# Performance work log

Hardware: AMD Instinct MI355X
Metric: run time of the kernel (lower is better)

Reference implementation:

```python
import jax, jax.numpy as jnp
import numpy as np

EMBED = 1024
HEADS = 16
HEAD_DIM = EMBED // HEADS


def setup_inputs() -> dict:
    key = jax.random.key(0)
    ks = jax.random.split(key, 9)
    s = 0.02
    return {
        "hidden_states": jax.random.normal(ks[0], (1, 4, 1500, EMBED), dtype=jnp.float32),
        "q_w": jax.random.normal(ks[1], (EMBED, EMBED), dtype=jnp.float32) * s,
        "q_b": jax.random.normal(ks[2], (EMBED,), dtype=jnp.float32) * s,
        "k_w": jax.random.normal(ks[3], (EMBED, EMBED), dtype=jnp.float32) * s,
        "v_w": jax.random.normal(ks[4], (EMBED, EMBED), dtype=jnp.float32) * s,
        "v_b": jax.random.normal(ks[5], (EMBED,), dtype=jnp.float32) * s,
        "out_w": jax.random.normal(ks[6], (EMBED, EMBED), dtype=jnp.float32) * s,
        "out_b": jax.random.normal(ks[7], (EMBED,), dtype=jnp.float32) * s,
    }


def reference(hidden_states, q_w, q_b, k_w, v_w, v_b, out_w, out_b):
    # hidden_states: [1, B, S, E]
    _, bsz, tgt_len, _ = hidden_states.shape
    x = hidden_states[0]  # [B, S, E]
    scaling = HEAD_DIM ** -0.5

    def split_heads(t):  # [B, S, E] -> [B, H, S, Dh]
        return t.reshape(bsz, tgt_len, HEADS, HEAD_DIM).transpose(0, 2, 1, 3)

    # Linear layers use torch convention: y = x @ W.T + b  (k_proj has no bias)
    q = split_heads((x @ q_w.T + q_b) * scaling)
    k = split_heads(x @ k_w.T)
    v = split_heads(x @ v_w.T + v_b)

    # attention scores [B, H, S, S]
    attn_weights = jnp.einsum("bhqd,bhkd->bhqk", q, k)
    attn_probs = jax.nn.softmax(attn_weights, axis=-1)
    attn_out = jnp.einsum("bhqk,bhkd->bhqd", attn_probs, v)  # [B, H, S, Dh]

    attn_out = attn_out.transpose(0, 2, 1, 3).reshape(1, bsz, tgt_len, EMBED)
    return attn_out @ out_w.T + out_b
```

## Files before the change

### kernel.cpp

```cpp
#include <hip/hip_runtime.h>
#include <cstddef>
#include <cstdint>

#define EMB 1024
#define SEQ 1500
#define NB 4
#define NH 16
#define DH 64
#define MTOT (NB*SEQ)
#define VTS 1536

typedef __bf16 bf16;
typedef __bf16 bf16x4 __attribute__((ext_vector_type(4)));
typedef __bf16 bf16x8 __attribute__((ext_vector_type(8)));
typedef short  s16x4  __attribute__((ext_vector_type(4)));
typedef float  f32x4  __attribute__((ext_vector_type(4)));

#define LOG2E 1.44269504088896340736f

__device__ __forceinline__ void async16(const void* g, const void* l) {
    __builtin_amdgcn_global_load_lds(
        (const __attribute__((address_space(1))) uint32_t*)g,
        (__attribute__((address_space(3))) uint32_t*)l, 16, 0, 0);
}

__device__ __forceinline__ uint32_t pack_bf16_trunc(float e0, float e1) {
    return __builtin_amdgcn_perm(__builtin_bit_cast(uint32_t, e1),
                                 __builtin_bit_cast(uint32_t, e0), 0x07060302u);
}

struct CvtArgs {
    const float* xs; bf16* xd;
    const float* w[4]; bf16* wd[4];
};

__global__ __launch_bounds__(256) void cvt_kernel(CvtArgs a) {
    const size_t NX = (size_t)MTOT * EMB;
    const size_t NW = (size_t)EMB * EMB;
    const size_t tot = NX + 4 * NW;
    for (size_t i = ((size_t)blockIdx.x * 256 + threadIdx.x) * 4; i < tot;
         i += (size_t)gridDim.x * 1024) {
        const float* s; bf16* d; size_t off;
        if (i < NX) { s = a.xs; d = a.xd; off = i; }
        else {
            size_t j = i - NX;
            int wi = (int)(j >> 20);
            off = j & (NW - 1);
            s = a.w[wi]; d = a.wd[wi];
        }
        float4 v = *(const float4*)(s + off);
        bf16x4 o = { (bf16)v.x, (bf16)v.y, (bf16)v.z, (bf16)v.w };
        *(bf16x4*)(d + off) = o;
    }
}

__global__ __launch_bounds__(256) void gemm_fused(
    const bf16* __restrict__ X,
    const bf16* __restrict__ W0, const bf16* __restrict__ W1, const bf16* __restrict__ W2,
    const float* __restrict__ b_q, const float* __restrict__ b_v,
    bf16* __restrict__ Oq, bf16* __restrict__ Ok, bf16* __restrict__ Ovt,
    int M)
{
    __shared__ bf16 As[2][128 * 32];
    __shared__ bf16 Bs[2][128 * 32];
    const int tid = threadIdx.x;
    const int lane = tid & 63, w = tid >> 6;
    const int q = lane >> 4, lr = lane & 15;
    const int wr = w >> 1, wc = w & 1;

    const int id = blockIdx.x;
    const int t_ = id >> 3;
    const int mtile = (id & 7) + (t_ % 6) * 8;
    const int y = t_ / 6;
    const int m0 = mtile * 128;
    const int proj = y >> 3;
    const int n0 = (y & 7) * 128;

    const bf16 *PA, *PB;
    int baseA, baseB, limA, limB;
    if (proj == 2) {
        PA = X;  baseA = m0; limA = M;
        PB = W2; baseB = n0; limB = EMB;
    } else {
        PA = (proj == 0) ? W0 : W1;
        baseA = n0; limA = EMB;
        PB = X; baseB = m0; limB = M;
    }

    f32x4 acc[4][4] = {};

    const int srow = w * 32 + (lane >> 2);
    const int swz_ch = (((lane & 3) ^ ((lane >> 3) & 3))) * 8;
    const bf16* pA[2]; const bf16* pB[2];
#pragma unroll
    for (int i = 0; i < 2; i++) {
        int ra = baseA + srow + i * 16; ra = ra < limA ? ra : limA - 1;
        int rb = baseB + srow + i * 16; rb = rb < limB ? rb : limB - 1;
        pA[i] = PA + (size_t)ra * EMB + swz_ch;
        pB[i] = PB + (size_t)rb * EMB + swz_ch;
    }

#pragma unroll
    for (int i = 0; i < 2; i++) {
        async16(pA[i], As[0] + (w * 2 + i) * 512);
        async16(pB[i], Bs[0] + (w * 2 + i) * 512);
    }

    const int qsw = (q ^ ((lr >> 1) & 3)) * 8;
    const int arow = (wr * 64 + lr) * 32;
    const int brow = (wc * 64 + lr) * 32;

    for (int k0 = 0; k0 < EMB; k0 += 32) {
        const int cur = (k0 >> 5) & 1;
        __syncthreads();
        const int nxt = k0 + 32;
        if (nxt < EMB) {
#pragma unroll
            for (int i = 0; i < 2; i++) {
                async16(pA[i] + nxt, As[cur ^ 1] + (w * 2 + i) * 512);
                async16(pB[i] + nxt, Bs[cur ^ 1] + (w * 2 + i) * 512);
            }
        }
        const bf16* Ab = As[cur];
        const bf16* Bb = Bs[cur];
        bf16x8 af[4], bfr[4];
#pragma unroll
        for (int t = 0; t < 4; t++) {
            af[t]  = *(const bf16x8*)(Ab + arow + t * 512 + qsw);
            bfr[t] = *(const bf16x8*)(Bb + brow + t * 512 + qsw);
        }
#pragma unroll
        for (int ti = 0; ti < 4; ti++)
#pragma unroll
            for (int tj = 0; tj < 4; tj++)
                acc[ti][tj] = __builtin_amdgcn_mfma_f32_16x16x32_bf16(
                    af[ti], bfr[tj], acc[ti][tj], 0, 0, 0);
    }

    if (proj <= 1) {
        const float scale = (proj == 0) ? 0.125f * LOG2E : 1.0f;
        const float* bias = (proj == 0) ? b_q : nullptr;
        bf16* O = (proj == 0) ? Oq : Ok;
#pragma unroll
        for (int tj = 0; tj < 4; tj++) {
            const int m = m0 + wc * 64 + tj * 16 + lr;
            if (m >= M) continue;
            const int b_ = m / SEQ, s_ = m % SEQ;
#pragma unroll
            for (int ti = 0; ti < 4; ti++) {
                const int nb = n0 + wr * 64 + ti * 16 + q * 4;
                const int h = nb >> 6, d = nb & 63;
                float4 b4 = bias ? *(const float4*)(bias + nb)
                                 : make_float4(0.f, 0.f, 0.f, 0.f);
                bf16x4 o;
                o[0] = (bf16)((acc[ti][tj][0] + b4.x) * scale);
                o[1] = (bf16)((acc[ti][tj][1] + b4.y) * scale);
                o[2] = (bf16)((acc[ti][tj][2] + b4.z) * scale);
                o[3] = (bf16)((acc[ti][tj][3] + b4.w) * scale);
                *(bf16x4*)(O + (((size_t)b_ * NH + h) * SEQ + s_) * DH + d) = o;
            }
        }
    } else {
#pragma unroll
        for (int ti = 0; ti < 4; ti++) {
            const int mb = m0 + wr * 64 + ti * 16 + q * 4;
            if (mb >= M) continue;
            const int b_ = mb / SEQ, s_ = mb % SEQ;
#pragma unroll
            for (int tj = 0; tj < 4; tj++) {
                const int nb = n0 + wc * 64 + tj * 16 + lr;
                const int h = nb >> 6, d = nb & 63;
                const float bv = b_v[nb];
                bf16x4 o;
                o[0] = (bf16)(acc[ti][tj][0] + bv);
                o[1] = (bf16)(acc[ti][tj][1] + bv);
                o[2] = (bf16)(acc[ti][tj][2] + bv);
                o[3] = (bf16)(acc[ti][tj][3] + bv);
                *(bf16x4*)(Ovt + ((size_t)(b_ * NH + h) * DH + d) * VTS + s_) = o;
            }
        }
    }
}

__global__ __launch_bounds__(256) void gemm_out64(
    const bf16* __restrict__ X, const bf16* __restrict__ Wo,
    const float* __restrict__ b_o, float* __restrict__ Of, int M)
{
    __shared__ bf16 Ws[2][128 * 32];
    __shared__ bf16 Xs[2][64 * 32];
    const int tid = threadIdx.x;
    const int lane = tid & 63, w = tid >> 6;
    const int q = lane >> 4, lr = lane & 15;
    const int wm = w & 1, wn = w >> 1;
    const int m0 = blockIdx.x * 64, n0 = blockIdx.y * 128;

    const int srow = tid >> 2;
    const int sch8 = ((tid & 3) ^ ((tid >> 3) & 3)) * 8;
    int xr = m0 + srow; if (xr >= M) xr = M - 1;
    const bf16* pX  = X  + (size_t)xr * EMB + sch8;
    const bf16* pW0 = Wo + (size_t)(n0 + srow) * EMB + sch8;
    const bf16* pW1 = Wo + (size_t)(n0 + 64 + srow) * EMB + sch8;

    async16(pW0, Ws[0] + tid * 8);
    async16(pW1, Ws[0] + tid * 8 + 2048);
    async16(pX,  Xs[0] + tid * 8);

    f32x4 acc[4][2] = {};
    const int fsw = (q ^ ((lr >> 1) & 3)) * 8;

    for (int k0 = 0; k0 < EMB; k0 += 32) {
        const int cur = (k0 >> 5) & 1;
        __syncthreads();
        if (k0 + 32 < EMB) {
            async16(pW0 + k0 + 32, Ws[cur ^ 1] + tid * 8);
            async16(pW1 + k0 + 32, Ws[cur ^ 1] + tid * 8 + 2048);
            async16(pX  + k0 + 32, Xs[cur ^ 1] + tid * 8);
        }
        bf16x8 wf[4], xf[2];
#pragma unroll
        for (int t = 0; t < 4; t++)
            wf[t] = *(const bf16x8*)(Ws[cur] + (wn * 64 + t * 16 + lr) * 32 + fsw);
#pragma unroll
        for (int t = 0; t < 2; t++)
            xf[t] = *(const bf16x8*)(Xs[cur] + (wm * 32 + t * 16 + lr) * 32 + fsw);
#pragma unroll
        for (int ti = 0; ti < 4; ti++)
#pragma unroll
            for (int tj = 0; tj < 2; tj++)
                acc[ti][tj] = __builtin_amdgcn_mfma_f32_16x16x32_bf16(
                    wf[ti], xf[tj], acc[ti][tj], 0, 0, 0);
    }

#pragma unroll
    for (int tj = 0; tj < 2; tj++) {
        const int m = m0 + wm * 32 + tj * 16 + lr;
        if (m >= M) continue;
#pragma unroll
        for (int ti = 0; ti < 4; ti++) {
            const int nb = n0 + wn * 64 + ti * 16 + q * 4;
            const float4 b4 = *(const float4*)(b_o + nb);
            float4 o;
            o.x = acc[ti][tj][0] + b4.x;
            o.y = acc[ti][tj][1] + b4.y;
            o.z = acc[ti][tj][2] + b4.z;
            o.w = acc[ti][tj][3] + b4.w;
            *(float4*)(Of + (size_t)m * EMB + nb) = o;
        }
    }
}

__global__ __launch_bounds__(256) void attn_mfma(
    const bf16* __restrict__ Qb, const bf16* __restrict__ Kb,
    const bf16* __restrict__ Vt, bf16* __restrict__ ctx)
{
    __shared__ bf16 Ks[2][64 * 64];
    __shared__ bf16 Vs[2][64 * 64];
    const int tid = threadIdx.x;
    const int lane = tid & 63, w = tid >> 6;
    const int q = lane >> 4, lr = lane & 15;
    const int bh = blockIdx.x, b_ = bh >> 4, h_ = bh & 15;
    const int q0 = blockIdx.y * 128;
    const size_t base = (size_t)bh * SEQ * DH;
    const size_t vbase = (size_t)bh * DH * VTS;

    int qrow[2];
    bf16x8 qf[2][2];
#pragma unroll
    for (int g = 0; g < 2; g++) {
        qrow[g] = q0 + g * 64 + w * 16 + lr;
        const int qrc = qrow[g] < SEQ ? qrow[g] : (SEQ - 1);
        qf[g][0] = *(const bf16x8*)(Qb + base + (size_t)qrc * DH + q * 8);
        qf[g][1] = *(const bf16x8*)(Qb + base + (size_t)qrc * DH + 32 + q * 8);
    }

    f32x4 oacc[2][4] = {};
    f32x4 lacc[2] = {};
    const s16x4 ones = { (short)0x3F80, (short)0x3F80, (short)0x3F80, (short)0x3F80 };

    const int srow = tid >> 3;
    const int sch8 = ((tid & 7) ^ (srow & 7)) * 8;
    const int kswz = lr & 7;

    const int NT = (SEQ + 63) / 64;

    {
        int r0 = srow, r1 = srow + 32;
        async16(Kb + base + (size_t)r0 * DH + sch8, Ks[0] + tid * 8);
        async16(Kb + base + (size_t)r1 * DH + sch8, Ks[0] + tid * 8 + 2048);
        async16(Vt + vbase + (size_t)srow * VTS + sch8,        Vs[0] + tid * 8);
        async16(Vt + vbase + (size_t)(srow + 32) * VTS + sch8, Vs[0] + tid * 8 + 2048);
    }

    for (int kt = 0; kt < NT; kt++) {
        const int k0 = kt * 64;
        const int cur = kt & 1;
        __syncthreads();

        if (kt + 1 < NT) {
            const int kn = k0 + 64;
            int r0 = kn + srow;      if (r0 >= SEQ) r0 = SEQ - 1;
            int r1 = kn + srow + 32; if (r1 >= SEQ) r1 = SEQ - 1;
            async16(Kb + base + (size_t)r0 * DH + sch8, Ks[cur ^ 1] + tid * 8);
            async16(Kb + base + (size_t)r1 * DH + sch8, Ks[cur ^ 1] + tid * 8 + 2048);
            async16(Vt + vbase + (size_t)srow * VTS + kn + sch8,
                    Vs[cur ^ 1] + tid * 8);
            async16(Vt + vbase + (size_t)(srow + 32) * VTS + kn + sch8,
                    Vs[cur ^ 1] + tid * 8 + 2048);
        }

        const bf16* Kc = Ks[cur];
        const bf16* Vc = Vs[cur];

        bf16x8 kf[2][4];
#pragma unroll
        for (int s = 0; s < 2; s++)
#pragma unroll
            for (int mt = 0; mt < 4; mt++)
                kf[s][mt] = *(const bf16x8*)(Kc + (mt * 16 + lr) * 64 +
                                             ((4 * s + q) ^ kswz) * 8);

        s16x4 pf[2][4];
#pragma unroll
        for (int g = 0; g < 2; g++) {
            f32x4 st[4] = {};
#pragma unroll
            for (int s = 0; s < 2; s++)
#pragma unroll
                for (int mt = 0; mt < 4; mt++)
                    st[mt] = __builtin_amdgcn_mfma_f32_16x16x32_bf16(
                        kf[s][mt], qf[g][s], st[mt], 0, 0, 0);

            if (k0 + 64 > SEQ) {
#pragma unroll
                for (int mt = 0; mt < 4; mt++)
#pragma unroll
                    for (int r = 0; r < 4; r++)
                        if (k0 + mt * 16 + q * 4 + r >= SEQ) st[mt][r] = -16384.0f;
            }

#pragma unroll
            for (int mt = 0; mt < 4; mt++) {
                float e0 = __builtin_amdgcn_exp2f(st[mt][0]);
                float e1 = __builtin_amdgcn_exp2f(st[mt][1]);
                float e2 = __builtin_amdgcn_exp2f(st[mt][2]);
                float e3 = __builtin_amdgcn_exp2f(st[mt][3]);
                uint32_t lo = pack_bf16_trunc(e0, e1);
                uint32_t hi = pack_bf16_trunc(e2, e3);
                uint2 pk = { lo, hi };
                pf[g][mt] = __builtin_bit_cast(s16x4, pk);
            }
#pragma unroll
            for (int c = 0; c < 4; c++)
                lacc[g] = __builtin_amdgcn_mfma_f32_16x16x16bf16_1k(
                    ones, pf[g][c], lacc[g], 0, 0, 0);
        }

#pragma unroll
        for (int c = 0; c < 4; c++) {
#pragma unroll
            for (int dt = 0; dt < 4; dt++) {
                const s16x4 vf = __builtin_bit_cast(s16x4,
                    *(const bf16x4*)(Vc + (dt * 16 + lr) * 64 +
                                     ((2 * c + (q >> 1)) ^ kswz) * 8 + (q & 1) * 4));
                oacc[0][dt] = __builtin_amdgcn_mfma_f32_16x16x16bf16_1k(
                    vf, pf[0][c], oacc[0][dt], 0, 0, 0);
                oacc[1][dt] = __builtin_amdgcn_mfma_f32_16x16x16bf16_1k(
                    vf, pf[1][c], oacc[1][dt], 0, 0, 0);
            }
        }
    }

#pragma unroll
    for (int g = 0; g < 2; g++) {
        const float inv = 1.0f / lacc[g][0];
        if (qrow[g] < SEQ) {
            const size_t rowoff = ((size_t)b_ * SEQ + qrow[g]) * EMB + h_ * DH;
#pragma unroll
            for (int dt = 0; dt < 4; dt++) {
                bf16x4 o;
#pragma unroll
                for (int r = 0; r < 4; r++) o[r] = (bf16)(oacc[g][dt][r] * inv);
                *(bf16x4*)(ctx + rowoff + dt * 16 + q * 4) = o;
            }
        }
    }
}

extern "C" void kernel_launch(void* const* d_in, const int* in_sizes, int n_in,
                              void* d_out, int out_size, void* d_ws, size_t ws_size,
                              hipStream_t stream) {
    const float* x     = (const float*)d_in[0];
    const float* q_w   = (const float*)d_in[1];
    const float* q_b   = (const float*)d_in[2];
    const float* k_w   = (const float*)d_in[3];
    const float* v_w   = (const float*)d_in[4];
    const float* v_b   = (const float*)d_in[5];
    const float* out_w = (const float*)d_in[6];
    const float* out_b = (const float*)d_in[7];
    float* out = (float*)d_out;

    const size_t nbuf = (size_t)MTOT * EMB;
    const size_t nvt  = (size_t)NB * NH * DH * VTS;
    const size_t nw   = (size_t)EMB * EMB;
    bf16* xb  = (bf16*)d_ws;
    bf16* qws = xb  + nbuf;
    bf16* kws = qws + nbuf;
    bf16* vtw = kws + nbuf;
    bf16* wqb = vtw + nvt;
    bf16* wkb = wqb + nw;
    bf16* wvb = wkb + nw;
    bf16* wob = wvb + nw;
    bf16* ctx = xb;

    CvtArgs ca;
    ca.xs = x;      ca.xd = xb;
    ca.w[0] = q_w;  ca.wd[0] = wqb;
    ca.w[1] = k_w;  ca.wd[1] = wkb;
    ca.w[2] = v_w;  ca.wd[2] = wvb;
    ca.w[3] = out_w; ca.wd[3] = wob;
    cvt_kernel<<<dim3(2560), 256, 0, stream>>>(ca);

    gemm_fused<<<dim3(48 * 24), 256, 0, stream>>>(
        xb, wqb, wkb, wvb, q_b, v_b, qws, kws, vtw, MTOT);

    attn_mfma<<<dim3(NB * NH, (SEQ + 127) / 128), 256, 0, stream>>>(qws, kws, vtw, ctx);

    gemm_out64<<<dim3((MTOT + 63) / 64, 8), 256, 0, stream>>>(ctx, wob, out_b, out, MTOT);
}
```

Measured before the change: 240.6 us.

## Rewrite projection GEMMs as single-wave blocks with vmcnt-based double buffering

The QKV and output projection GEMMs are rewritten so that each block is a single 64-thread wavefront owning a 64x128 (or 64x64) tile. Because the block has one wave, __syncthreads is no longer needed and the loop waits on its own async loads with s_waitcnt vmcnt. Block IDs are remapped so that tiles sharing the same weight rows fall on the same XCD. This aims to remove barrier overhead and improve L2 locality, at the cost of less LDS reuse per block, many more small blocks, and higher per-wave register pressure from the larger accumulator.

```diff
diff --git a/kernel.cpp b/kernel.cpp
--- a/kernel.cpp
+++ b/kernel.cpp
@@ -54,87 +54,84 @@
     }
 }
 
-__global__ __launch_bounds__(256) void gemm_fused(
+__global__ __launch_bounds__(64) void gemm_sw_qkv(
     const bf16* __restrict__ X,
     const bf16* __restrict__ W0, const bf16* __restrict__ W1, const bf16* __restrict__ W2,
     const float* __restrict__ b_q, const float* __restrict__ b_v,
-    bf16* __restrict__ Oq, bf16* __restrict__ Ok, bf16* __restrict__ Ovt,
-    int M)
+    bf16* __restrict__ Oq, bf16* __restrict__ Ok, bf16* __restrict__ Ovt, int M)
 {
-    __shared__ bf16 As[2][128 * 32];
+    __shared__ bf16 As[2][64 * 32];
     __shared__ bf16 Bs[2][128 * 32];
     const int tid = threadIdx.x;
-    const int lane = tid & 63, w = tid >> 6;
-    const int q = lane >> 4, lr = lane & 15;
-    const int wr = w >> 1, wc = w & 1;
+    const int q = tid >> 4, lr = tid & 15;
 
     const int id = blockIdx.x;
-    const int t_ = id >> 3;
-    const int mtile = (id & 7) + (t_ % 6) * 8;
-    const int y = t_ / 6;
-    const int m0 = mtile * 128;
-    const int proj = y >> 3;
-    const int n0 = (y & 7) * 128;
+    const int proj = id / 768;
+    const int rid = id - proj * 768;
+    const int xcd = rid & 7;
+    const int h = rid >> 3;
 
     const bf16 *PA, *PB;
     int baseA, baseB, limA, limB;
+    int atile, btile;
+    if (proj < 2) { atile = h / 6;  btile = (h % 6) * 8 + xcd; }
+    else          { atile = h / 12; btile = (h % 12) * 8 + xcd; }
     if (proj == 2) {
-        PA = X;  baseA = m0; limA = M;
-        PB = W2; baseB = n0; limB = EMB;
+        PA = X;  baseA = btile * 64;  limA = M;
+        PB = W2; baseB = atile * 128; limB = EMB;
     } else {
         PA = (proj == 0) ? W0 : W1;
-        baseA = n0; limA = EMB;
-        PB = X; baseB = m0; limB = M;
-    }
-
-    f32x4 acc[4][4] = {};
-
-    const int srow = w * 32 + (lane >> 2);
-    const int swz_ch = (((lane & 3) ^ ((lane >> 3) & 3))) * 8;
-    const bf16* pA[2]; const bf16* pB[2];
-#pragma unroll
-    for (int i = 0; i < 2; i++) {
-        int ra = baseA + srow + i * 16; ra = ra < limA ? ra : limA - 1;
-        int rb = baseB + srow + i * 16; rb = rb < limB ? rb : limB - 1;
-        pA[i] = PA + (size_t)ra * EMB + swz_ch;
-        pB[i] = PB + (size_t)rb * EMB + swz_ch;
-    }
-
-#pragma unroll
-    for (int i = 0; i < 2; i++) {
-        async16(pA[i], As[0] + (w * 2 + i) * 512);
-        async16(pB[i], Bs[0] + (w * 2 + i) * 512);
-    }
-
+        baseA = atile * 64;  limA = EMB;
+        PB = X; baseB = btile * 128; limB = M;
+    }
+
+    const int cs = ((tid & 3) ^ ((tid >> 3) & 3)) * 8;
+    const bf16* pA[4];
+    const bf16* pB[8];
+#pragma unroll
+    for (int i = 0; i < 4; i++) {
+        int r = baseA + i * 16 + (tid >> 2); r = r < limA ? r : limA - 1;
+        pA[i] = PA + (size_t)r * EMB + cs;
+    }
+#pragma unroll
+    for (int i = 0; i < 8; i++) {
+        int r = baseB + i * 16 + (tid >> 2); r = r < limB ? r : limB - 1;
+        pB[i] = PB + (size_t)r * EMB + cs;
+    }
+
+#pragma unroll
+    for (int i = 0; i < 4; i++) async16(pA[i], &As[0][i * 512]);
+#pragma unroll
+    for (int i = 0; i < 8; i++) async16(pB[i], &Bs[0][i * 512]);
+
+    f32x4 acc[4][8] = {};
     const int qsw = (q ^ ((lr >> 1) & 3)) * 8;
-    const int arow = (wr * 64 + lr) * 32;
-    const int brow = (wc * 64 + lr) * 32;
-
-    for (int k0 = 0; k0 < EMB; k0 += 32) {
-        const int cur = (k0 >> 5) & 1;
-        __syncthreads();
-        const int nxt = k0 + 32;
-        if (nxt < EMB) {
-#pragma unroll
-            for (int i = 0; i < 2; i++) {
-                async16(pA[i] + nxt, As[cur ^ 1] + (w * 2 + i) * 512);
-                async16(pB[i] + nxt, Bs[cur ^ 1] + (w * 2 + i) * 512);
-            }
-        }
-        const bf16* Ab = As[cur];
-        const bf16* Bb = Bs[cur];
-        bf16x8 af[4], bfr[4];
-#pragma unroll
-        for (int t = 0; t < 4; t++) {
-            af[t]  = *(const bf16x8*)(Ab + arow + t * 512 + qsw);
-            bfr[t] = *(const bf16x8*)(Bb + brow + t * 512 + qsw);
-        }
+
+    for (int kt = 0; kt < 32; kt++) {
+        const int cur = kt & 1;
+        if (kt < 31) {
+            const int kn = (kt + 1) * 32;
+#pragma unroll
+            for (int i = 0; i < 4; i++) async16(pA[i] + kn, &As[cur ^ 1][i * 512]);
+#pragma unroll
+            for (int i = 0; i < 8; i++) async16(pB[i] + kn, &Bs[cur ^ 1][i * 512]);
+            asm volatile("s_waitcnt vmcnt(12)" ::: "memory");
+        } else {
+            asm volatile("s_waitcnt vmcnt(0)" ::: "memory");
+        }
+        bf16x8 af[4], bfv[8];
+#pragma unroll
+        for (int t = 0; t < 4; t++)
+            af[t] = *(const bf16x8*)&As[cur][(t * 16 + lr) * 32 + qsw];
+#pragma unroll
+        for (int t = 0; t < 8; t++)
+            bfv[t] = *(const bf16x8*)&Bs[cur][(t * 16 + lr) * 32 + qsw];
 #pragma unroll
         for (int ti = 0; ti < 4; ti++)
 #pragma unroll
-            for (int tj = 0; tj < 4; tj++)
+            for (int tj = 0; tj < 8; tj++)
                 acc[ti][tj] = __builtin_amdgcn_mfma_f32_16x16x32_bf16(
-                    af[ti], bfr[tj], acc[ti][tj], 0, 0, 0);
+                    af[ti], bfv[tj], acc[ti][tj], 0, 0, 0);
     }
 
     if (proj <= 1) {
@@ -142,14 +139,14 @@
         const float* bias = (proj == 0) ? b_q : nullptr;
         bf16* O = (proj == 0) ? Oq : Ok;
 #pragma unroll
-        for (int tj = 0; tj < 4; tj++) {
-            const int m = m0 + wc * 64 + tj * 16 + lr;
+        for (int tj = 0; tj < 8; tj++) {
+            const int m = btile * 128 + tj * 16 + lr;
             if (m >= M) continue;
             const int b_ = m / SEQ, s_ = m % SEQ;
 #pragma unroll
             for (int ti = 0; ti < 4; ti++) {
-                const int nb = n0 + wr * 64 + ti * 16 + q * 4;
-                const int h = nb >> 6, d = nb & 63;
+                const int dg = ti * 16 + q * 4;
+                const int nb = atile * 64 + dg;
                 float4 b4 = bias ? *(const float4*)(bias + nb)
                                  : make_float4(0.f, 0.f, 0.f, 0.f);
                 bf16x4 o;
@@ -157,87 +154,98 @@
                 o[1] = (bf16)((acc[ti][tj][1] + b4.y) * scale);
                 o[2] = (bf16)((acc[ti][tj][2] + b4.z) * scale);
                 o[3] = (bf16)((acc[ti][tj][3] + b4.w) * scale);
-                *(bf16x4*)(O + (((size_t)b_ * NH + h) * SEQ + s_) * DH + d) = o;
+                *(bf16x4*)(O + (((size_t)b_ * NH + atile) * SEQ + s_) * DH + dg) = o;
             }
         }
     } else {
 #pragma unroll
         for (int ti = 0; ti < 4; ti++) {
-            const int mb = m0 + wr * 64 + ti * 16 + q * 4;
+            const int mb = btile * 64 + ti * 16 + q * 4;
             if (mb >= M) continue;
             const int b_ = mb / SEQ, s_ = mb % SEQ;
 #pragma unroll
-            for (int tj = 0; tj < 4; tj++) {
-                const int nb = n0 + wc * 64 + tj * 16 + lr;
-                const int h = nb >> 6, d = nb & 63;
-                const float bv = b_v[nb];
+            for (int tj = 0; tj < 8; tj++) {
+                const int d = atile * 128 + tj * 16 + lr;
+                const int hh = d >> 6, dd = d & 63;
+                const float bv = b_v[d];
                 bf16x4 o;
                 o[0] = (bf16)(acc[ti][tj][0] + bv);
                 o[1] = (bf16)(acc[ti][tj][1] + bv);
                 o[2] = (bf16)(acc[ti][tj][2] + bv);
                 o[3] = (bf16)(acc[ti][tj][3] + bv);
-                *(bf16x4*)(Ovt + ((size_t)(b_ * NH + h) * DH + d) * VTS + s_) = o;
-            }
-        }
-    }
-}
-
-__global__ __launch_bounds__(256) void gemm_out64(
+                *(bf16x4*)(Ovt + ((size_t)(b_ * NH + hh) * DH + dd) * VTS + s_) = o;
+            }
+        }
+    }
+}
+
+__global__ __launch_bounds__(64) void gemm_sw_out(
     const bf16* __restrict__ X, const bf16* __restrict__ Wo,
     const float* __restrict__ b_o, float* __restrict__ Of, int M)
 {
-    __shared__ bf16 Ws[2][128 * 32];
-    __shared__ bf16 Xs[2][64 * 32];
+    __shared__ bf16 As[2][64 * 32];
+    __shared__ bf16 Bs[2][64 * 32];
     const int tid = threadIdx.x;
-    const int lane = tid & 63, w = tid >> 6;
-    const int q = lane >> 4, lr = lane & 15;
-    const int wm = w & 1, wn = w >> 1;
-    const int m0 = blockIdx.x * 64, n0 = blockIdx.y * 128;
-
-    const int srow = tid >> 2;
-    const int sch8 = ((tid & 3) ^ ((tid >> 3) & 3)) * 8;
-    int xr = m0 + srow; if (xr >= M) xr = M - 1;
-    const bf16* pX  = X  + (size_t)xr * EMB + sch8;
-    const bf16* pW0 = Wo + (size_t)(n0 + srow) * EMB + sch8;
-    const bf16* pW1 = Wo + (size_t)(n0 + 64 + srow) * EMB + sch8;
-
-    async16(pW0, Ws[0] + tid * 8);
-    async16(pW1, Ws[0] + tid * 8 + 2048);
-    async16(pX,  Xs[0] + tid * 8);
-
-    f32x4 acc[4][2] = {};
-    const int fsw = (q ^ ((lr >> 1) & 3)) * 8;
-
-    for (int k0 = 0; k0 < EMB; k0 += 32) {
-        const int cur = (k0 >> 5) & 1;
-        __syncthreads();
-        if (k0 + 32 < EMB) {
-            async16(pW0 + k0 + 32, Ws[cur ^ 1] + tid * 8);
-            async16(pW1 + k0 + 32, Ws[cur ^ 1] + tid * 8 + 2048);
-            async16(pX  + k0 + 32, Xs[cur ^ 1] + tid * 8);
-        }
-        bf16x8 wf[4], xf[2];
-#pragma unroll
-        for (int t = 0; t < 4; t++)
-            wf[t] = *(const bf16x8*)(Ws[cur] + (wn * 64 + t * 16 + lr) * 32 + fsw);
-#pragma unroll
-        for (int t = 0; t < 2; t++)
-            xf[t] = *(const bf16x8*)(Xs[cur] + (wm * 32 + t * 16 + lr) * 32 + fsw);
+    const int q = tid >> 4, lr = tid & 15;
+
+    const int id = blockIdx.x;
+    const int xcd = id & 7;
+    const int h = id >> 3;
+    const int atile = h / 12;
+    const int btile = (h % 12) * 8 + xcd;
+
+    const int cs = ((tid & 3) ^ ((tid >> 3) & 3)) * 8;
+    const bf16* pA[4];
+    const bf16* pB[4];
+#pragma unroll
+    for (int i = 0; i < 4; i++) {
+        int ra = atile * 64 + i * 16 + (tid >> 2);
+        pA[i] = Wo + (size_t)ra * EMB + cs;
+        int rb = btile * 64 + i * 16 + (tid >> 2); rb = rb < M ? rb : M - 1;
+        pB[i] = X + (size_t)rb * EMB + cs;
+    }
+
+#pragma unroll
+    for (int i = 0; i < 4; i++) async16(pA[i], &As[0][i * 512]);
+#pragma unroll
+    for (int i = 0; i < 4; i++) async16(pB[i], &Bs[0][i * 512]);
+
+    f32x4 acc[4][4] = {};
+    const int qsw = (q ^ ((lr >> 1) & 3)) * 8;
+
+    for (int kt = 0; kt < 32; kt++) {
+        const int cur = kt & 1;
+        if (kt < 31) {
+            const int kn = (kt + 1) * 32;
+#pragma unroll
+            for (int i = 0; i < 4; i++) async16(pA[i] + kn, &As[cur ^ 1][i * 512]);
+#pragma unroll
+            for (int i = 0; i < 4; i++) async16(pB[i] + kn, &Bs[cur ^ 1][i * 512]);
+            asm volatile("s_waitcnt vmcnt(8)" ::: "memory");
+        } else {
+            asm volatile("s_waitcnt vmcnt(0)" ::: "memory");
+        }
+        bf16x8 af[4], bfv[4];
+#pragma unroll
+        for (int t = 0; t < 4; t++) {
+            af[t]  = *(const bf16x8*)&As[cur][(t * 16 + lr) * 32 + qsw];
+            bfv[t] = *(const bf16x8*)&Bs[cur][(t * 16 + lr) * 32 + qsw];
+        }
 #pragma unroll
         for (int ti = 0; ti < 4; ti++)
 #pragma unroll
-            for (int tj = 0; tj < 2; tj++)
+            for (int tj = 0; tj < 4; tj++)
                 acc[ti][tj] = __builtin_amdgcn_mfma_f32_16x16x32_bf16(
-                    wf[ti], xf[tj], acc[ti][tj], 0, 0, 0);
-    }
-
-#pragma unroll
-    for (int tj = 0; tj < 2; tj++) {
-        const int m = m0 + wm * 32 + tj * 16 + lr;
+                    af[ti], bfv[tj], acc[ti][tj], 0, 0, 0);
+    }
+
+#pragma unroll
+    for (int tj = 0; tj < 4; tj++) {
+        const int m = btile * 64 + tj * 16 + lr;
         if (m >= M) continue;
 #pragma unroll
         for (int ti = 0; ti < 4; ti++) {
-            const int nb = n0 + wn * 64 + ti * 16 + q * 4;
+            const int nb = atile * 64 + ti * 16 + q * 4;
             const float4 b4 = *(const float4*)(b_o + nb);
             float4 o;
             o.x = acc[ti][tj][0] + b4.x;
@@ -420,10 +428,10 @@
     ca.w[3] = out_w; ca.wd[3] = wob;
     cvt_kernel<<<dim3(2560), 256, 0, stream>>>(ca);
 
-    gemm_fused<<<dim3(48 * 24), 256, 0, stream>>>(
+    gemm_sw_qkv<<<dim3(2304), 64, 0, stream>>>(
         xb, wqb, wkb, wvb, q_b, v_b, qws, kws, vtw, MTOT);
 
     attn_mfma<<<dim3(NB * NH, (SEQ + 127) / 128), 256, 0, stream>>>(qws, kws, vtw, ctx);
 
-    gemm_out64<<<dim3((MTOT + 63) / 64, 8), 256, 0, stream>>>(ctx, wob, out_b, out, MTOT);
-}
+    gemm_sw_out<<<dim3(1536), 64, 0, stream>>>(ctx, wob, out_b, out, MTOT);
+}
```

Measured after the change: 286.0 us. +18.8%, slower.

## Retile output projection to 128x64 tiles with XCD-aware block mapping

Applied to the files above, without the earlier changes.

The output-projection GEMM now uses 128-row activation tiles by 64-column weight tiles instead of 64x128, launched as a flat 1D grid of 768 blocks. Each block id is remapped so that consecutive blocks on the same XCD share weight tiles, aiming for better L2 locality across the chiplets. The larger M tile halves how often the activation rows are re-read per weight tile. It keeps the same per-block LDS size and MFMA count, but the hard-coded mapping (6×8 M-tiles, 16 N-tiles) assumes the fixed problem shape.

```diff
diff --git a/kernel.cpp b/kernel.cpp
--- a/kernel.cpp
+++ b/kernel.cpp
@@ -182,62 +182,76 @@
     }
 }
 
-__global__ __launch_bounds__(256) void gemm_out64(
+__global__ __launch_bounds__(256) void gemm_out(
     const bf16* __restrict__ X, const bf16* __restrict__ Wo,
     const float* __restrict__ b_o, float* __restrict__ Of, int M)
 {
-    __shared__ bf16 Ws[2][128 * 32];
-    __shared__ bf16 Xs[2][64 * 32];
+    __shared__ bf16 As[2][64 * 32];
+    __shared__ bf16 Bs[2][128 * 32];
     const int tid = threadIdx.x;
     const int lane = tid & 63, w = tid >> 6;
     const int q = lane >> 4, lr = lane & 15;
-    const int wm = w & 1, wn = w >> 1;
-    const int m0 = blockIdx.x * 64, n0 = blockIdx.y * 128;
-
-    const int srow = tid >> 2;
-    const int sch8 = ((tid & 3) ^ ((tid >> 3) & 3)) * 8;
-    int xr = m0 + srow; if (xr >= M) xr = M - 1;
-    const bf16* pX  = X  + (size_t)xr * EMB + sch8;
-    const bf16* pW0 = Wo + (size_t)(n0 + srow) * EMB + sch8;
-    const bf16* pW1 = Wo + (size_t)(n0 + 64 + srow) * EMB + sch8;
-
-    async16(pW0, Ws[0] + tid * 8);
-    async16(pW1, Ws[0] + tid * 8 + 2048);
-    async16(pX,  Xs[0] + tid * 8);
-
-    f32x4 acc[4][2] = {};
-    const int fsw = (q ^ ((lr >> 1) & 3)) * 8;
+    const int wc = w & 1, wr = w >> 1;
+
+    const int id = blockIdx.x;
+    const int xcd = id & 7;
+    const int h = id >> 3;
+    const int mtile = (h % 6) * 8 + xcd;
+    const int ntile = h / 6;
+    const int m0 = mtile * 128, n0 = ntile * 64;
+
+    const int cs = ((tid & 3) ^ ((tid >> 3) & 3)) * 8;
+    const bf16* pA = Wo + (size_t)(n0 + (tid >> 2)) * EMB + cs;
+    const int srow = w * 32 + (lane >> 2);
+    const bf16* pB[2];
+#pragma unroll
+    for (int i = 0; i < 2; i++) {
+        int rb = m0 + srow + i * 16; rb = rb < M ? rb : M - 1;
+        pB[i] = X + (size_t)rb * EMB + cs;
+    }
+
+    async16(pA, As[0] + w * 512);
+#pragma unroll
+    for (int i = 0; i < 2; i++)
+        async16(pB[i], Bs[0] + (w * 2 + i) * 512);
+
+    f32x4 acc[2][4] = {};
+    const int qsw = (q ^ ((lr >> 1) & 3)) * 8;
+    const int arow = (wr * 32 + lr) * 32;
+    const int brow = (wc * 64 + lr) * 32;
 
     for (int k0 = 0; k0 < EMB; k0 += 32) {
         const int cur = (k0 >> 5) & 1;
         __syncthreads();
-        if (k0 + 32 < EMB) {
-            async16(pW0 + k0 + 32, Ws[cur ^ 1] + tid * 8);
-            async16(pW1 + k0 + 32, Ws[cur ^ 1] + tid * 8 + 2048);
-            async16(pX  + k0 + 32, Xs[cur ^ 1] + tid * 8);
-        }
-        bf16x8 wf[4], xf[2];
+        const int nxt = k0 + 32;
+        if (nxt < EMB) {
+            async16(pA + nxt, As[cur ^ 1] + w * 512);
+#pragma unroll
+            for (int i = 0; i < 2; i++)
+                async16(pB[i] + nxt, Bs[cur ^ 1] + (w * 2 + i) * 512);
+        }
+        bf16x8 af[2], bfr[4];
+#pragma unroll
+        for (int t = 0; t < 2; t++)
+            af[t] = *(const bf16x8*)(As[cur] + arow + t * 512 + qsw);
 #pragma unroll
         for (int t = 0; t < 4; t++)
-            wf[t] = *(const bf16x8*)(Ws[cur] + (wn * 64 + t * 16 + lr) * 32 + fsw);
-#pragma unroll
-        for (int t = 0; t < 2; t++)
-            xf[t] = *(const bf16x8*)(Xs[cur] + (wm * 32 + t * 16 + lr) * 32 + fsw);
-#pragma unroll
-        for (int ti = 0; ti < 4; ti++)
-#pragma unroll
-            for (int tj = 0; tj < 2; tj++)
+            bfr[t] = *(const bf16x8*)(Bs[cur] + brow + t * 512 + qsw);
+#pragma unroll
+        for (int ti = 0; ti < 2; ti++)
+#pragma unroll
+            for (int tj = 0; tj < 4; tj++)
                 acc[ti][tj] = __builtin_amdgcn_mfma_f32_16x16x32_bf16(
-                    wf[ti], xf[tj], acc[ti][tj], 0, 0, 0);
-    }
-
-#pragma unroll
-    for (int tj = 0; tj < 2; tj++) {
-        const int m = m0 + wm * 32 + tj * 16 + lr;
+                    af[ti], bfr[tj], acc[ti][tj], 0, 0, 0);
+    }
+
+#pragma unroll
+    for (int tj = 0; tj < 4; tj++) {
+        const int m = m0 + wc * 64 + tj * 16 + lr;
         if (m >= M) continue;
 #pragma unroll
-        for (int ti = 0; ti < 4; ti++) {
-            const int nb = n0 + wn * 64 + ti * 16 + q * 4;
+        for (int ti = 0; ti < 2; ti++) {
+            const int nb = n0 + wr * 32 + ti * 16 + q * 4;
             const float4 b4 = *(const float4*)(b_o + nb);
             float4 o;
             o.x = acc[ti][tj][0] + b4.x;
@@ -425,5 +439,5 @@
 
     attn_mfma<<<dim3(NB * NH, (SEQ + 127) / 128), 256, 0, stream>>>(qws, kws, vtw, ctx);
 
-    gemm_out64<<<dim3((MTOT + 63) / 64, 8), 256, 0, stream>>>(ctx, wob, out_b, out, MTOT);
-}
+    gemm_out<<<dim3(768), 256, 0, stream>>>(ctx, wob, out_b, out, MTOT);
+}
```

Result: no change. 241.3 us (+0.3%).
